# Kernel tuning notes

Measured on AMD Instinct MI355X. Metric: run time of the kernel, lower is better.

Reference implementation:

```python
import jax, jax.numpy as jnp
import numpy as np

N = 32          # agents_num
IN_DIM = 16     # node feature dim (excluding 2 pos cols)
HID = 128
HEADS = 4
OUT = 5
DUEL_H = 256
RADIUS = 0.3
LATENT = HID + HID * HEADS * 2  # 1152
BS = 128


def _lin(k, i, o):
    s = 1.0 / np.sqrt(i)
    return jax.random.uniform(k, (i, o), minval=-s, maxval=s, dtype=jnp.float32)


def setup_inputs() -> dict:
    key = jax.random.key(0)
    ks = jax.random.split(key, 16)
    pos = jax.random.uniform(ks[0], (BS, N, 2))
    feats = jax.random.normal(ks[1], (BS, N, IN_DIM))
    aidx = jax.random.randint(ks[2], (BS,), 0, N).astype(jnp.float32)
    node = jnp.concatenate([pos, feats], axis=-1).reshape(BS, N * (2 + IN_DIM))
    obs = jnp.concatenate([node, aidx[:, None]], axis=1)  # (BS, N*(2+IN_DIM)+1)
    return {
        "obs": obs,
        "enc_w1": _lin(ks[3], IN_DIM, HID), "enc_b1": jnp.zeros((HID,)),
        "enc_w2": _lin(ks[4], HID, HID), "enc_b2": jnp.zeros((HID,)),
        "wl1": _lin(ks[5], HID, HEADS * HID), "wr1": _lin(ks[6], HID, HEADS * HID),
        "att1": jax.random.normal(ks[7], (HEADS, HID)) * 0.1, "bias1": jnp.zeros((HEADS * HID,)),
        "wl2": _lin(ks[8], HID * HEADS, HEADS * HID), "wr2": _lin(ks[9], HID * HEADS, HEADS * HID),
        "att2": jax.random.normal(ks[10], (HEADS, HID)) * 0.1, "bias2": jnp.zeros((HEADS * HID,)),
        "q_w1": _lin(ks[11], LATENT, DUEL_H), "q_b1": jnp.zeros((DUEL_H,)),
        "q_w2": _lin(ks[12], DUEL_H, OUT), "q_b2": jnp.zeros((OUT,)),
        "v_w1": _lin(ks[13], LATENT, DUEL_H), "v_b1": jnp.zeros((DUEL_H,)),
        "v_w2": _lin(ks[14], DUEL_H, 1), "v_b2": jnp.zeros((1,)),
    }


def _gatv2(x, adj, wl, wr, att, bias):
    # Dense-masked GATv2 (PyG semantics: lin_l on source j, lin_r on target i,
    # leaky_relu(x_i + x_j) . att, softmax over neighbors j, aggregate lin_l(x_j)).
    bs, n, _ = x.shape
    gl = (x @ wl).reshape(bs, n, HEADS, HID)  # source transform
    gr = (x @ wr).reshape(bs, n, HEADS, HID)  # target transform
    e = jax.nn.leaky_relu(gr[:, :, None] + gl[:, None, :], 0.2)  # [b, i, j, h, c]
    logits = jnp.einsum('bijhc,hc->bijh', e, att)
    logits = jnp.where(adj[..., None], logits, -jnp.inf)  # diag always True (self loops)
    alpha = jax.nn.softmax(logits, axis=2)
    out = jnp.einsum('bijh,bjhc->bihc', alpha, gl).reshape(bs, n, HEADS * HID)
    return out + bias


def reference(obs, enc_w1, enc_b1, enc_w2, enc_b2,
              wl1, wr1, att1, bias1, wl2, wr2, att2, bias2,
              q_w1, q_b1, q_w2, q_b2, v_w1, v_b1, v_w2, v_b2):
    bs = obs.shape[0]
    node = obs[:, :-1].reshape(bs, N, 2 + IN_DIM)
    pos, feats = node[..., :2], node[..., 2:]
    aidx = jnp.clip(obs[:, -1], 0, N - 1).astype(jnp.int32)

    # radius_graph (per-graph, loop=False) + GATv2 add_self_loops => diag True
    d2 = jnp.sum((pos[:, :, None] - pos[:, None, :]) ** 2, axis=-1)  # [bs, N, N]
    adj = (d2 < RADIUS ** 2) | jnp.eye(N, dtype=bool)

    # encoder MLP then ReLU (as in forward)
    h = jax.nn.relu(feats @ enc_w1 + enc_b1)
    x = jax.nn.relu(h @ enc_w2 + enc_b2)  # [bs, N, HID]

    b = jnp.arange(bs)
    x1 = x[b, aidx]  # [bs, HID]

    x = jax.nn.relu(_gatv2(x, adj, wl1, wr1, att1, bias1))  # [bs, N, HID*HEADS]
    x2 = x[b, aidx]

    x = jax.nn.relu(_gatv2(x, adj, wl2, wr2, att2, bias2))
    x3 = x[b, aidx]

    x_cat = jnp.concatenate([x1, x2, x3], axis=1)  # [bs, LATENT]

    q = jax.nn.relu(x_cat @ q_w1 + q_b1) @ q_w2 + q_b2  # [bs, OUT]
    v = jax.nn.relu(x_cat @ v_w1 + v_b1) @ v_w2 + v_b2  # [bs, 1]
    return q - q.mean(axis=1, keepdims=True) + v
```

## Files before the change

kernel.cpp:

```cpp
#include <hip/hip_runtime.h>
#include <hip/hip_bf16.h>

typedef unsigned int uint_t;
typedef unsigned short ushort_t;
typedef __attribute__((ext_vector_type(8))) short short8;
typedef __attribute__((ext_vector_type(4))) float floatx4;

__device__ __forceinline__ float4 fma4(float4 a, float s, float4 w){
  a.x += s*w.x; a.y += s*w.y; a.z += s*w.z; a.w += s*w.w; return a;
}
__device__ __forceinline__ float4 relu4(float4 a){
  return make_float4(fmaxf(a.x,0.f),fmaxf(a.y,0.f),fmaxf(a.z,0.f),fmaxf(a.w,0.f));
}
__device__ __forceinline__ unsigned bf16rne(float f){
  unsigned u = __float_as_uint(f);
  return (u + 0x7fffu + ((u>>16)&1u)) >> 16;
}
__device__ __forceinline__ uint_t packbf(float f){
  unsigned hb = bf16rne(f);
  float hf = __uint_as_float(hb<<16);
  unsigned lb = bf16rne(f - hf);
  return (hb<<16) | lb;
}
__device__ __forceinline__ uint4 pack4(float4 v){
  uint4 u; u.x=packbf(v.x); u.y=packbf(v.y); u.z=packbf(v.z); u.w=packbf(v.w); return u;
}
__device__ __forceinline__ float unpk(uint_t u){
  return __uint_as_float(u & 0xffff0000u) + __uint_as_float(u<<16);
}
#define UNPACK8(u0,u1,hi,lo) \
  hi[0]=(short)(u0.x>>16); lo[0]=(short)u0.x; \
  hi[1]=(short)(u0.y>>16); lo[1]=(short)u0.y; \
  hi[2]=(short)(u0.z>>16); lo[2]=(short)u0.z; \
  hi[3]=(short)(u0.w>>16); lo[3]=(short)u0.w; \
  hi[4]=(short)(u1.x>>16); lo[4]=(short)u1.x; \
  hi[5]=(short)(u1.y>>16); lo[5]=(short)u1.y; \
  hi[6]=(short)(u1.z>>16); lo[6]=(short)u1.z; \
  hi[7]=(short)(u1.w>>16); lo[7]=(short)u1.w;


template<int NKC>
__device__ __forceinline__ void hgemm_body(
    const uint_t* __restrict__ xcatpk,
    const ushort_t* __restrict__ qw1Thi, const ushort_t* __restrict__ qw1Tlo,
    const ushort_t* __restrict__ vw1Thi, const ushort_t* __restrict__ vw1Tlo,
    float* __restrict__ part, int ks, int ct, int t, int k0c, int slot0)
{
  const int w = t>>6, lane = t&63, m = lane&15, quad = lane>>4;
  const ushort_t* Bhi = (ct<4) ? qw1Thi : vw1Thi;
  const int cbl = (ct<4) ? ct*64 : (ct-4)*64;
  const int cbg = (ct<4) ? ct*64 : 256 + (ct-4)*64;
  const int kb = k0c + ks*NKC;
  const uint_t* ap = xcatpk + (size_t)w*18432 + m*32 + quad*8 + (size_t)kb*512;
  const ushort_t* bp0 = Bhi + (size_t)((cbl>>4)+0)*18432 + m*32 + quad*8 + (size_t)kb*512;
  const ushort_t* bp1 = Bhi + (size_t)((cbl>>4)+1)*18432 + m*32 + quad*8 + (size_t)kb*512;
  const ushort_t* bp2 = Bhi + (size_t)((cbl>>4)+2)*18432 + m*32 + quad*8 + (size_t)kb*512;
  const ushort_t* bp3 = Bhi + (size_t)((cbl>>4)+3)*18432 + m*32 + quad*8 + (size_t)kb*512;
  const size_t lod = (size_t)(qw1Tlo - qw1Thi);
  floatx4 acc[4];
  #pragma unroll
  for (int i=0;i<4;i++) acc[i] = (floatx4){0.f,0.f,0.f,0.f};
  #pragma unroll
  for (int kc=0; kc<NKC; kc++){
    const uint4 ua0 = *(const uint4*)(ap);
    const uint4 ua1 = *(const uint4*)(ap+4);
    ap += 512;
    short8 ahi, alo;
    UNPACK8(ua0,ua1,ahi,alo)
    const ushort_t* bps[4] = {bp0, bp1, bp2, bp3};
    #pragma unroll
    for (int nt=0; nt<4; nt++){
      const short8 bh = *(const short8*)(bps[nt] + kc*512);
      const short8 bl = *(const short8*)(bps[nt] + kc*512 + lod);
      acc[nt] = __builtin_amdgcn_mfma_f32_16x16x32_bf16(ahi, bh, acc[nt], 0,0,0);
      acc[nt] = __builtin_amdgcn_mfma_f32_16x16x32_bf16(ahi, bl, acc[nt], 0,0,0);
      acc[nt] = __builtin_amdgcn_mfma_f32_16x16x32_bf16(alo, bh, acc[nt], 0,0,0);
    }
  }
  float* pdst = part + (size_t)(slot0+ks)*65536;
  const int crow0 = w*16 + quad*4;
  #pragma unroll
  for (int nt=0; nt<4; nt++){
    const int col = cbg + nt*16 + m;
    #pragma unroll
    for (int r=0;r<4;r++)
      pdst[(size_t)(crow0 + r)*512 + col] = acc[nt][r];
  }
}

__global__ __launch_bounds__(256) void prep_kernel(
    const float* __restrict__ obs,
    const float* __restrict__ enc_w1, const float* __restrict__ enc_b1,
    const float* __restrict__ enc_w2, const float* __restrict__ enc_b2,
    const float* __restrict__ wl1, const float* __restrict__ wr1,
    const float* __restrict__ wl2, const float* __restrict__ wr2,
    const float* __restrict__ q_w1, const float* __restrict__ v_w1,
    ushort_t* __restrict__ wl1Thi, ushort_t* __restrict__ wl1Tlo,
    ushort_t* __restrict__ wr1Thi, ushort_t* __restrict__ wr1Tlo,
    ushort_t* __restrict__ wl2Thi, ushort_t* __restrict__ wl2Tlo,
    ushort_t* __restrict__ wr2Thi, ushort_t* __restrict__ wr2Tlo,
    ushort_t* __restrict__ qw1Thi, ushort_t* __restrict__ qw1Tlo,
    ushort_t* __restrict__ vw1Thi, ushort_t* __restrict__ vw1Tlo,
    uint_t* __restrict__ xpk, uint_t* __restrict__ xcatpk,
    unsigned* __restrict__ adjw, int* __restrict__ aiw)
{
  const int t = threadIdx.x, bid = blockIdx.x;
  if (bid >= 512){
    __shared__ float sm[32][33];
    const int cw = bid - 512;
    const float* in; ushort_t* ohi; ushort_t* olo; int K, N, tt, ktiles;
    if (cw < 64)       { in=wl1;  ohi=wl1Thi; olo=wl1Tlo; K=128;  N=512; tt=cw;     ktiles=4;  }
    else if (cw < 128) { in=wr1;  ohi=wr1Thi; olo=wr1Tlo; K=128;  N=512; tt=cw-64;  ktiles=4;  }
    else if (cw < 384) { in=wl2;  ohi=wl2Thi; olo=wl2Tlo; K=512;  N=512; tt=cw-128; ktiles=16; }
    else if (cw < 640) { in=wr2;  ohi=wr2Thi; olo=wr2Tlo; K=512;  N=512; tt=cw-384; ktiles=16; }
    else if (cw < 800) { in=q_w1; ohi=qw1Thi; olo=qw1Tlo; K=1152; N=256; tt=cw-640; ktiles=20; }
    else               { in=v_w1; ohi=vw1Thi; olo=vw1Tlo; K=1152; N=256; tt=cw-800; ktiles=20; }
    const int kt = tt % ktiles, nt = tt / ktiles;
    const int r = t>>5, c = t&31;
    #pragma unroll
    for (int i=0;i<4;i++)
      sm[r+i*8][c] = in[(size_t)(kt*32 + r + i*8)*N + nt*32 + c];
    __syncthreads();
    #pragma unroll
    for (int i=0;i<4;i++){
      const int nl = r + i*8;
      const int n  = nt*32 + nl;
      const float f = sm[c][nl];
      const unsigned hb = bf16rne(f);
      const float hf = __uint_as_float(hb<<16);
      const unsigned lb = bf16rne(f - hf);
      const size_t off = (size_t)(n>>4)*(size_t)(16*K) + (size_t)kt*512 + (size_t)(n&15)*32 + c;
      ohi[off] = (ushort_t)hb;
      olo[off] = (ushort_t)lb;
    }
    return;
  }
  __shared__ float s_pos[64];
  __shared__ float s_feats[128];
  __shared__ __align__(16) float s_h[8*132];
  __shared__ int s_ai;
  const int s = bid & 127, g = bid >> 7;
  const float* ob = obs + s*577;

  if (t==0){
    float a = ob[576];
    a = fminf(fmaxf(a, 0.f), 31.f);
    s_ai = (int)a;
    if (g==0) aiw[s] = (int)a;
  }
  if (t < 128){ const int n=t>>4, f=t&15; s_feats[t] = ob[(g*8+n)*18+2+f]; }
  if (g==0 && t>=128 && t<192){ const int u=t-128; s_pos[u] = ob[(u>>1)*18 + (u&1)]; }
  __syncthreads();

  if (g==0 && t < 32){
    const float px = s_pos[2*t], py = s_pos[2*t+1];
    const float R2 = 0.09f;
    unsigned mm = 0u;
    for (int j=0;j<32;j++){
      const float dx = __fsub_rn(px, s_pos[2*j]), dy = __fsub_rn(py, s_pos[2*j+1]);
      const float d2 = __fadd_rn(__fmul_rn(dx,dx), __fmul_rn(dy,dy));
      if (d2 <= R2 || j==t) mm |= (1u<<j);
    }
    adjw[s*32+t] = mm;
  }

  const int n = t>>5, c0 = (t&31)*4;
  {
    float4 a = *(const float4*)(enc_b1+c0);
    #pragma unroll
    for (int f=0; f<16; f++)
      a = fma4(a, s_feats[n*16+f], *(const float4*)(enc_w1 + f*128 + c0));
    *(float4*)&s_h[n*132+c0] = relu4(a);
  }
  __syncthreads();
  {
    float4 a = *(const float4*)(enc_b2+c0);
    #pragma unroll 4
    for (int k=0;k<128;k+=4){
      const float4 hv = *(const float4*)&s_h[n*132+k];
      a = fma4(a, hv.x, *(const float4*)(enc_w2 + (k+0)*128 + c0));
      a = fma4(a, hv.y, *(const float4*)(enc_w2 + (k+1)*128 + c0));
      a = fma4(a, hv.z, *(const float4*)(enc_w2 + (k+2)*128 + c0));
      a = fma4(a, hv.w, *(const float4*)(enc_w2 + (k+3)*128 + c0));
    }
    a = relu4(a);
    const uint4 p = pack4(a);
    const int i = g*8 + n;
    uint_t* xp = xpk + (size_t)(s*2 + (i>>4))*2048 + (c0>>5)*512 + (i&15)*32 + (c0&31);
    *(uint4*)xp = p;
    if (i == s_ai){
      uint_t* xc = xcatpk + (size_t)(s>>4)*18432 + (c0>>5)*512 + (s&15)*32 + (c0&31);
      *(uint4*)xc = p;
    }
  }
}

__global__ __launch_bounds__(512) void pa1_kernel(
    const uint_t* __restrict__ xpk,
    const ushort_t* __restrict__ wl1Thi, const ushort_t* __restrict__ wl1Tlo,
    const ushort_t* __restrict__ wr1Thi, const ushort_t* __restrict__ wr1Tlo,
    const float* __restrict__ att, const float* __restrict__ bias,
    const unsigned* __restrict__ adjw, const int* __restrict__ aiw,
    uint_t* __restrict__ x2pk, uint_t* __restrict__ xcatpk)
{
  __shared__ __align__(16) uint_t s_ax[4096];
  __shared__ __align__(16) float s_gl[32*132];
  __shared__ __align__(16) float s_gr[32*132];
  __shared__ __align__(16) float s_att[128];
  __shared__ __align__(16) float s_b[128];
  __shared__ float s_lg[32*33];
  __shared__ unsigned s_adj[32];
  const int t = threadIdx.x, bid = blockIdx.x;

  const int s = bid & 127, h = bid >> 7;
  const int w = t>>6, lane = t&63, m = lane&15, quad = lane>>4;
  const int mat = w>>2, cpair = w&3;

  if (t < 128){ s_att[t] = att[h*128 + t]; s_b[t] = bias[h*128 + t]; }
  if (t >= 224 && t < 256) s_adj[t-224] = adjw[s*32 + (t-224)];
  const int ai = aiw[s];

  #pragma unroll
  for (int j=0;j<2;j++){
    const int W = t*8 + j*4;
    const int kcl = W>>10, rp = (W>>9)&1, u = W&511;
    const int du = u ^ (((u>>5)&7)<<2);
    *(uint4*)&s_ax[kcl*1024 + rp*512 + du] =
      *(const uint4*)(xpk + (size_t)(s*2+rp)*2048 + (size_t)kcl*512 + u);
  }

  const ushort_t* Bhi = (mat==0) ? wl1Thi : wr1Thi;
  const ushort_t* Blo = (mat==0) ? wl1Tlo : wr1Tlo;
  const int nbase = h*8 + cpair*2;
  const ushort_t* bp0 = Bhi + (size_t)(nbase+0)*2048 + m*32 + quad*8;
  const ushort_t* bp1 = Bhi + (size_t)(nbase+1)*2048 + m*32 + quad*8;
  const size_t lod = (size_t)(Blo - Bhi);
  const int sw = (m*32 + quad*8) ^ ((m&7)<<2);
  floatx4 acc[2][2];
  #pragma unroll
  for (int i=0;i<2;i++)
    #pragma unroll
    for (int j=0;j<2;j++) acc[i][j] = (floatx4){0.f,0.f,0.f,0.f};

  __syncthreads();

  #pragma unroll
  for (int kc=0; kc<4; kc++){
    const uint4 u00 = *(const uint4*)&s_ax[kc*1024 + sw];
    const uint4 u01 = *(const uint4*)&s_ax[kc*1024 + (sw^4)];
    const uint4 u10 = *(const uint4*)&s_ax[kc*1024 + 512 + sw];
    const uint4 u11 = *(const uint4*)&s_ax[kc*1024 + 512 + (sw^4)];
    short8 ahi0, alo0, ahi1, alo1;
    UNPACK8(u00,u01,ahi0,alo0)
    UNPACK8(u10,u11,ahi1,alo1)
    const ushort_t* bps[2] = {bp0, bp1};
    #pragma unroll
    for (int nt=0; nt<2; nt++){
      const short8 bh = *(const short8*)(bps[nt] + kc*512);
      const short8 bl = *(const short8*)(bps[nt] + kc*512 + lod);
      acc[0][nt] = __builtin_amdgcn_mfma_f32_16x16x32_bf16(ahi0, bh, acc[0][nt], 0,0,0);
      acc[0][nt] = __builtin_amdgcn_mfma_f32_16x16x32_bf16(ahi0, bl, acc[0][nt], 0,0,0);
      acc[0][nt] = __builtin_amdgcn_mfma_f32_16x16x32_bf16(alo0, bh, acc[0][nt], 0,0,0);
      acc[1][nt] = __builtin_amdgcn_mfma_f32_16x16x32_bf16(ahi1, bh, acc[1][nt], 0,0,0);
      acc[1][nt] = __builtin_amdgcn_mfma_f32_16x16x32_bf16(ahi1, bl, acc[1][nt], 0,0,0);
      acc[1][nt] = __builtin_amdgcn_mfma_f32_16x16x32_bf16(alo1, bh, acc[1][nt], 0,0,0);
    }
  }
  {
    float* dst = mat ? s_gr : s_gl;
    const int colbase = cpair*32;
    #pragma unroll
    for (int nt=0; nt<2; nt++){
      const int col = colbase + nt*16 + m;
      #pragma unroll
      for (int r=0;r<4;r++){
        dst[(quad*4+r)*132 + col]      = acc[0][nt][r];
        dst[(16+quad*4+r)*132 + col]   = acc[1][nt][r];
      }
    }
  }
  __syncthreads();

  {
    const int i = t>>4, jb = t&15;
    float lacc[2] = {0.f,0.f};
    for (int c=0;c<128;c+=4){
      const float4 g = *(const float4*)&s_gr[i*132+c];
      const float4 a = *(const float4*)&s_att[c];
      #pragma unroll
      for (int mm=0;mm<2;mm++){
        const float4 gj = *(const float4*)&s_gl[(jb+16*mm)*132 + c];
        float ex = g.x+gj.x; ex = fmaxf(ex, 0.2f*ex);
        float ey = g.y+gj.y; ey = fmaxf(ey, 0.2f*ey);
        float ez = g.z+gj.z; ez = fmaxf(ez, 0.2f*ez);
        float ew = g.w+gj.w; ew = fmaxf(ew, 0.2f*ew);
        lacc[mm] += ex*a.x + ey*a.y + ez*a.z + ew*a.w;
      }
    }
    s_lg[i*33 + jb]      = lacc[0];
    s_lg[i*33 + jb + 16] = lacc[1];
  }
  __syncthreads();

  #pragma unroll
  for (int rnd=0; rnd<2; rnd++){
    const int i = rnd*16 + (t>>5), j = t&31;
    const float lg = s_lg[i*33+j];
    const bool ok = (s_adj[i]>>j)&1u;
    float v = ok ? lg : -3.0e38f;
    #pragma unroll
    for (int d_=16; d_; d_>>=1) v = fmaxf(v, __shfl_xor(v, d_, 32));
    const float e = ok ? __expf(lg - v) : 0.f;
    float sum = e;
    #pragma unroll
    for (int d_=16; d_; d_>>=1) sum += __shfl_xor(sum, d_, 32);
    s_lg[i*33+j] = e / sum;
  }
  __syncthreads();

  {
    const int i = t>>4, c0 = (t&15)*8;
    float4 o0 = make_float4(0.f,0.f,0.f,0.f), o1 = o0;
    for (int j=0;j<32;j++){
      const float al = s_lg[i*33+j];
      o0 = fma4(o0, al, *(const float4*)&s_gl[j*132 + c0]);
      o1 = fma4(o1, al, *(const float4*)&s_gl[j*132 + c0 + 4]);
    }
    const float4 b0 = *(const float4*)&s_b[c0];
    const float4 b1 = *(const float4*)&s_b[c0+4];
    o0 = relu4(make_float4(o0.x+b0.x, o0.y+b0.y, o0.z+b0.z, o0.w+b0.w));
    o1 = relu4(make_float4(o1.x+b1.x, o1.y+b1.y, o1.z+b1.z, o1.w+b1.w));
    const uint4 p0 = pack4(o0), p1 = pack4(o1);
    const int kb = h*128 + c0;
    uint_t* xp = x2pk + (size_t)(s*2 + (i>>4))*8192 + (kb>>5)*512 + (i&15)*32 + (kb&31);
    *(uint4*)&xp[0] = p0;
    *(uint4*)&xp[4] = p1;
    if (i == ai){
      const int kk = 128 + kb;
      uint_t* tp = xcatpk + (size_t)(s>>4)*18432 + (kk>>5)*512 + (s&15)*32 + (kk&31);
      *(uint4*)&tp[0] = p0;
      *(uint4*)&tp[4] = p1;
    }
  }
}

__global__ __launch_bounds__(512) void gr2_kernel(
    const uint_t* __restrict__ xcatpk,
    const ushort_t* __restrict__ wr2Thi, const ushort_t* __restrict__ wr2Tlo,
    const ushort_t* __restrict__ qw1Thi, const ushort_t* __restrict__ qw1Tlo,
    const ushort_t* __restrict__ vw1Thi, const ushort_t* __restrict__ vw1Tlo,
    float* __restrict__ hpart, float* __restrict__ GR)
{
  const int t = threadIdx.x, bid = blockIdx.x;
  if (bid >= 32){
    const int hk = bid - 32;
    hgemm_body<5>(xcatpk, qw1Thi, qw1Tlo, vw1Thi, vw1Tlo, hpart, hk>>3, hk&7, t, 0, 0);
    return;
  }
  const int w = t>>6, lane = t&63, m = lane&15, quad = lane>>4;
  const uint_t* ap = xcatpk + (size_t)w*18432 + m*32 + quad*8 + (size_t)4*512;
  const ushort_t* bp = wr2Thi + (size_t)bid*8192 + m*32 + quad*8;
  const size_t lod = (size_t)(wr2Tlo - wr2Thi);
  floatx4 acc = (floatx4){0.f,0.f,0.f,0.f};
  #pragma unroll 4
  for (int kc=0; kc<16; kc++){
    const uint4 ua0 = *(const uint4*)(ap + kc*512);
    const uint4 ua1 = *(const uint4*)(ap + kc*512 + 4);
    short8 ahi, alo;
    UNPACK8(ua0,ua1,ahi,alo)
    const short8 bh = *(const short8*)(bp + kc*512);
    const short8 bl = *(const short8*)(bp + kc*512 + lod);
    acc = __builtin_amdgcn_mfma_f32_16x16x32_bf16(ahi, bh, acc, 0,0,0);
    acc = __builtin_amdgcn_mfma_f32_16x16x32_bf16(ahi, bl, acc, 0,0,0);
    acc = __builtin_amdgcn_mfma_f32_16x16x32_bf16(alo, bh, acc, 0,0,0);
  }
  const int row0 = w*16 + quad*4, col = bid*16 + m;
  #pragma unroll
  for (int r=0;r<4;r++)
    GR[(size_t)(row0 + r)*512 + col] = acc[r];
}

__global__ __launch_bounds__(512) void pa2_kernel(
    const uint_t* __restrict__ x2pk,
    const ushort_t* __restrict__ wl2Thi, const ushort_t* __restrict__ wl2Tlo,
    const float* __restrict__ GR,
    const float* __restrict__ att2, const float* __restrict__ bias2,
    const unsigned* __restrict__ adjw, const int* __restrict__ aiw,
    float* __restrict__ X3)
{
  __shared__ __align__(16) uint_t s_a[8192];
  __shared__ __align__(16) float s_gl[32*132];
  __shared__ __align__(16) float s_p2[128];
  __shared__ __align__(16) float s_at[128];
  __shared__ __align__(16) float s_bb[128];
  __shared__ float s_lg[32];
  __shared__ float s_al[32];
  const int t = threadIdx.x, bid = blockIdx.x;
  const int s = bid & 127, h = bid >> 7;
  const int w = t>>6, lane = t&63, m = lane&15, quad = lane>>4;
  (void)lane;
  const int ai = aiw[s];
  const unsigned arow = adjw[s*32+ai];

  if (t < 128){
    s_p2[t] = GR[(size_t)s*512 + h*128 + t];
    s_at[t] = att2[h*128+t];
    s_bb[t] = bias2[h*128+t];
  }

  const ushort_t* bq = wl2Thi + (size_t)(h*8 + w)*8192 + m*32 + quad*8;
  const size_t lod = (size_t)(wl2Tlo - wl2Thi);
  const int sw = (m*32 + quad*8) ^ ((m&7)<<2);
  floatx4 acc0 = (floatx4){0.f,0.f,0.f,0.f}, acc1 = acc0;

  #pragma unroll
  for (int half=0; half<2; half++){
    #pragma unroll
    for (int j=0;j<4;j++){
      const int W = t*16 + j*4;
      const int kcl = W>>10, rp = (W>>9)&1, u = W&511;
      const int du = u ^ (((u>>5)&7)<<2);
      *(uint4*)&s_a[kcl*1024 + rp*512 + du] =
        *(const uint4*)(x2pk + (size_t)(s*2+rp)*8192 + (size_t)(half*8+kcl)*512 + u);
    }
    __syncthreads();
    #pragma unroll 4
    for (int kcl=0; kcl<8; kcl++){
      const int kc = half*8 + kcl;
      const uint4 u00 = *(const uint4*)&s_a[kcl*1024 + sw];
      const uint4 u01 = *(const uint4*)&s_a[kcl*1024 + (sw^4)];
      const uint4 u10 = *(const uint4*)&s_a[kcl*1024 + 512 + sw];
      const uint4 u11 = *(const uint4*)&s_a[kcl*1024 + 512 + (sw^4)];
      short8 ahi0, alo0, ahi1, alo1;
      UNPACK8(u00,u01,ahi0,alo0)
      UNPACK8(u10,u11,ahi1,alo1)
      const short8 bh = *(const short8*)(bq + kc*512);
      const short8 bl = *(const short8*)(bq + kc*512 + lod);
      acc0 = __builtin_amdgcn_mfma_f32_16x16x32_bf16(ahi0, bh, acc0, 0,0,0);
      acc0 = __builtin_amdgcn_mfma_f32_16x16x32_bf16(ahi0, bl, acc0, 0,0,0);
      acc0 = __builtin_amdgcn_mfma_f32_16x16x32_bf16(alo0, bh, acc0, 0,0,0);
      acc1 = __builtin_amdgcn_mfma_f32_16x16x32_bf16(ahi1, bh, acc1, 0,0,0);
      acc1 = __builtin_amdgcn_mfma_f32_16x16x32_bf16(ahi1, bl, acc1, 0,0,0);
      acc1 = __builtin_amdgcn_mfma_f32_16x16x32_bf16(alo1, bh, acc1, 0,0,0);
    }
    __syncthreads();
  }
  {
    const int col = w*16 + m;
    #pragma unroll
    for (int r=0;r<4;r++){
      s_gl[(quad*4+r)*132 + col]    = acc0[r];
      s_gl[(16+quad*4+r)*132 + col] = acc1[r];
    }
  }
  __syncthreads();

  if (t < 256){
    const int j = t>>3, pq = t&7;
    float sum = 0.f;
    #pragma unroll
    for (int q=0;q<4;q++){
      const int c = pq*16 + q*4;
      const float4 g = *(const float4*)&s_gl[j*132 + c];
      const float4 r = *(const float4*)&s_p2[c];
      const float4 a = *(const float4*)&s_at[c];
      float e0 = r.x+g.x; e0 = fmaxf(e0, 0.2f*e0);
      float e1 = r.y+g.y; e1 = fmaxf(e1, 0.2f*e1);
      float e2 = r.z+g.z; e2 = fmaxf(e2, 0.2f*e2);
      float e3 = r.w+g.w; e3 = fmaxf(e3, 0.2f*e3);
      sum += e0*a.x + e1*a.y + e2*a.z + e3*a.w;
    }
    sum += __shfl_xor(sum,1,64);
    sum += __shfl_xor(sum,2,64);
    sum += __shfl_xor(sum,4,64);
    if (pq==0) s_lg[j] = sum;
  }
  __syncthreads();
  if (t < 32){
    const float lg = s_lg[t];
    const bool ok = (arow>>t)&1u;
    float v = ok ? lg : -3.0e38f;
    #pragma unroll
    for (int d_=16; d_; d_>>=1) v = fmaxf(v, __shfl_xor(v, d_, 32));
    const float e = ok ? __expf(lg - v) : 0.f;
    float sm = e;
    #pragma unroll
    for (int d_=16; d_; d_>>=1) sm += __shfl_xor(sm, d_, 32);
    s_al[t] = e / sm;
  }
  __syncthreads();
  if (t < 128){
    float acc2 = 0.f;
    #pragma unroll 8
    for (int j=0;j<32;j++) acc2 += s_al[j] * s_gl[j*132 + t];
    X3[(size_t)s*512 + h*128 + t] = fmaxf(acc2 + s_bb[t], 0.f);
  }
}

__global__ __launch_bounds__(512) void hepi_kernel(
    const float* __restrict__ X3, const float* __restrict__ hpart,
    const float* __restrict__ q_w1, const float* __restrict__ q_b1,
    const float* __restrict__ q_w2, const float* __restrict__ q_b2,
    const float* __restrict__ v_w1, const float* __restrict__ v_b1,
    const float* __restrict__ v_w2, const float* __restrict__ v_b2,
    float* __restrict__ out)
{
  __shared__ __align__(16) float s_x3[512];
  __shared__ float s_p6[8*6];
  const int t = threadIdx.x, s = blockIdx.x;
  const int w = t>>6, lane = t&63;

  s_x3[t] = X3[(size_t)s*512 + t];
  __syncthreads();

  float val;
  {
    const int col = t & 255;
    float acc = (t < 256) ? q_b1[col] : v_b1[col];
    #pragma unroll
    for (int ks=0; ks<4; ks++)
      acc += hpart[(size_t)ks*65536 + (size_t)s*512 + t];
    const float* Wp = ((t < 256) ? q_w1 : v_w1) + (size_t)640*256 + col;
    #pragma unroll 8
    for (int k=0;k<512;k++) acc += s_x3[k] * Wp[(size_t)k*256];
    val = fmaxf(acc, 0.f);
  }

  float p[6];
  #pragma unroll
  for (int o=0;o<6;o++) p[o] = 0.f;
  if (t < 256){
    #pragma unroll
    for (int o=0;o<5;o++) p[o] = val * q_w2[t*5+o];
  } else {
    p[5] = val * v_w2[t-256];
  }
  #pragma unroll
  for (int d_=32; d_; d_>>=1){
    #pragma unroll
    for (int o=0;o<6;o++) p[o] += __shfl_xor(p[o], d_, 64);
  }
  if (lane==0){
    #pragma unroll
    for (int o=0;o<6;o++) s_p6[w*6+o] = p[o];
  }
  __syncthreads();
  if (t < 6){
    float v = 0.f;
    #pragma unroll
    for (int ww=0; ww<8; ww++) v += s_p6[ww*6 + t];
    s_p6[t] = v;
  }
  __syncthreads();
  if (t < 5){
    const float q0 = s_p6[0]+q_b2[0], q1 = s_p6[1]+q_b2[1], q2 = s_p6[2]+q_b2[2],
                q3 = s_p6[3]+q_b2[3], q4 = s_p6[4]+q_b2[4];
    const float mean = (q0+q1+q2+q3+q4) / 5.0f;
    const float v = s_p6[5] + v_b2[0];
    const float qt = (t==0?q0:t==1?q1:t==2?q2:t==3?q3:q4);
    out[s*5+t] = qt - mean + v;
  }
}

extern "C" void kernel_launch(void* const* d_in, const int* in_sizes, int n_in,
                              void* d_out, int out_size, void* d_ws, size_t ws_size,
                              hipStream_t stream) {
  (void)n_in; (void)out_size; (void)ws_size;
  const float* obs    = (const float*)d_in[0];
  const float* enc_w1 = (const float*)d_in[1];
  const float* enc_b1 = (const float*)d_in[2];
  const float* enc_w2 = (const float*)d_in[3];
  const float* enc_b2 = (const float*)d_in[4];
  const float* wl1    = (const float*)d_in[5];
  const float* wr1    = (const float*)d_in[6];
  const float* att1   = (const float*)d_in[7];
  const float* bias1  = (const float*)d_in[8];
  const float* wl2    = (const float*)d_in[9];
  const float* wr2    = (const float*)d_in[10];
  const float* att2   = (const float*)d_in[11];
  const float* bias2  = (const float*)d_in[12];
  const float* q_w1   = (const float*)d_in[13];
  const float* q_b1   = (const float*)d_in[14];
  const float* q_w2   = (const float*)d_in[15];
  const float* q_b2   = (const float*)d_in[16];
  const float* v_w1   = (const float*)d_in[17];
  const float* v_b1   = (const float*)d_in[18];
  const float* v_w2   = (const float*)d_in[19];
  const float* v_b2   = (const float*)d_in[20];

  char* ws = (char*)d_ws;
  uint_t*   x_pk    = (uint_t*)  (ws + 0);
  uint_t*   xcat_pk = (uint_t*)  (ws + 2097152);
  unsigned* adjw    = (unsigned*)(ws + 2686976);
  int*      aiw     = (int*)     (ws + 2703360);
  uint_t*   x2_pk   = (uint_t*)  (ws + 2703872);
  ushort_t* wl1Thi  = (ushort_t*)(ws + 11092480);
  ushort_t* wl1Tlo  = (ushort_t*)(ws + 11223552);
  ushort_t* wr1Thi  = (ushort_t*)(ws + 11354624);
  ushort_t* wr1Tlo  = (ushort_t*)(ws + 11485696);
  ushort_t* wl2Thi  = (ushort_t*)(ws + 11616768);
  ushort_t* wl2Tlo  = (ushort_t*)(ws + 12141056);
  ushort_t* qw1Thi  = (ushort_t*)(ws + 12665344);
  ushort_t* qw1Tlo  = (ushort_t*)(ws + 13255168);
  ushort_t* vw1Thi  = (ushort_t*)(ws + 13844992);
  ushort_t* vw1Tlo  = (ushort_t*)(ws + 14434816);
  ushort_t* wr2Thi  = (ushort_t*)(ws + 15024640);
  ushort_t* wr2Tlo  = (ushort_t*)(ws + 15548928);
  float*    GR      = (float*)   (ws + 16073216);
  float*    hpart   = (float*)   (ws + 16335360);
  float*    X3      = (float*)   (ws + 17383936);

  prep_kernel<<<512 + 960, 256, 0, stream>>>(obs, enc_w1, enc_b1, enc_w2, enc_b2,
      wl1, wr1, wl2, wr2, q_w1, v_w1,
      wl1Thi, wl1Tlo, wr1Thi, wr1Tlo, wl2Thi, wl2Tlo, wr2Thi, wr2Tlo,
      qw1Thi, qw1Tlo, vw1Thi, vw1Tlo,
      x_pk, xcat_pk, adjw, aiw);

  pa1_kernel<<<512, 512, 0, stream>>>(x_pk, wl1Thi, wl1Tlo, wr1Thi, wr1Tlo,
      att1, bias1, adjw, aiw, x2_pk, xcat_pk);

  gr2_kernel<<<64, 512, 0, stream>>>(xcat_pk, wr2Thi, wr2Tlo,
      qw1Thi, qw1Tlo, vw1Thi, vw1Tlo, hpart, GR);

  pa2_kernel<<<512, 512, 0, stream>>>(x2_pk, wl2Thi, wl2Tlo, GR,
      att2, bias2, adjw, aiw, X3);

  hepi_kernel<<<128, 512, 0, stream>>>(X3, hpart,
      q_w1, q_b1, q_w2, q_b2, v_w1, v_b1, v_w2, v_b2,
      (float*)d_out);
}
```

Measured before the change: 174.9 us.

## Fuse target-transform GEMM and head-split q/v layer into layer-2 attention kernel

Removes the separate gr2 kernel. Each pa2 block now computes its own 16-row tile of the wr2 target transform from xcat staged in shared memory. The 32 hgemm blocks move into the pa2 grid, so one launch and a global round trip disappear. The per-head slice of the q/v first-layer matvec also moves into pa2, writing per-head partials that a slimmer hepi kernel only sums. The cost is redundant work: each of the 16 samples in a row tile recomputes the same GR tile, and the fp32 weight reads for the q/v matvec are spread across many blocks.

```diff
diff --git a/kernel.cpp b/kernel.cpp
--- a/kernel.cpp
+++ b/kernel.cpp
@@ -344,49 +344,16 @@
   }
 }
 
-__global__ __launch_bounds__(512) void gr2_kernel(
-    const uint_t* __restrict__ xcatpk,
+__global__ __launch_bounds__(512) void pa2_kernel(
+    const uint_t* __restrict__ x2pk, const uint_t* __restrict__ xcatpk,
+    const ushort_t* __restrict__ wl2Thi, const ushort_t* __restrict__ wl2Tlo,
     const ushort_t* __restrict__ wr2Thi, const ushort_t* __restrict__ wr2Tlo,
     const ushort_t* __restrict__ qw1Thi, const ushort_t* __restrict__ qw1Tlo,
     const ushort_t* __restrict__ vw1Thi, const ushort_t* __restrict__ vw1Tlo,
-    float* __restrict__ hpart, float* __restrict__ GR)
-{
-  const int t = threadIdx.x, bid = blockIdx.x;
-  if (bid >= 32){
-    const int hk = bid - 32;
-    hgemm_body<5>(xcatpk, qw1Thi, qw1Tlo, vw1Thi, vw1Tlo, hpart, hk>>3, hk&7, t, 0, 0);
-    return;
-  }
-  const int w = t>>6, lane = t&63, m = lane&15, quad = lane>>4;
-  const uint_t* ap = xcatpk + (size_t)w*18432 + m*32 + quad*8 + (size_t)4*512;
-  const ushort_t* bp = wr2Thi + (size_t)bid*8192 + m*32 + quad*8;
-  const size_t lod = (size_t)(wr2Tlo - wr2Thi);
-  floatx4 acc = (floatx4){0.f,0.f,0.f,0.f};
-  #pragma unroll 4
-  for (int kc=0; kc<16; kc++){
-    const uint4 ua0 = *(const uint4*)(ap + kc*512);
-    const uint4 ua1 = *(const uint4*)(ap + kc*512 + 4);
-    short8 ahi, alo;
-    UNPACK8(ua0,ua1,ahi,alo)
-    const short8 bh = *(const short8*)(bp + kc*512);
-    const short8 bl = *(const short8*)(bp + kc*512 + lod);
-    acc = __builtin_amdgcn_mfma_f32_16x16x32_bf16(ahi, bh, acc, 0,0,0);
-    acc = __builtin_amdgcn_mfma_f32_16x16x32_bf16(ahi, bl, acc, 0,0,0);
-    acc = __builtin_amdgcn_mfma_f32_16x16x32_bf16(alo, bh, acc, 0,0,0);
-  }
-  const int row0 = w*16 + quad*4, col = bid*16 + m;
-  #pragma unroll
-  for (int r=0;r<4;r++)
-    GR[(size_t)(row0 + r)*512 + col] = acc[r];
-}
-
-__global__ __launch_bounds__(512) void pa2_kernel(
-    const uint_t* __restrict__ x2pk,
-    const ushort_t* __restrict__ wl2Thi, const ushort_t* __restrict__ wl2Tlo,
-    const float* __restrict__ GR,
     const float* __restrict__ att2, const float* __restrict__ bias2,
     const unsigned* __restrict__ adjw, const int* __restrict__ aiw,
-    float* __restrict__ X3)
+    const float* __restrict__ q_w1, const float* __restrict__ v_w1,
+    float* __restrict__ hpart, float* __restrict__ hp3)
 {
   __shared__ __align__(16) uint_t s_a[8192];
   __shared__ __align__(16) float s_gl[32*132];
@@ -396,21 +363,61 @@
   __shared__ float s_lg[32];
   __shared__ float s_al[32];
   const int t = threadIdx.x, bid = blockIdx.x;
+
+  if (bid >= 512){
+    const int hk = bid - 512;
+    hgemm_body<5>(xcatpk, qw1Thi, qw1Tlo, vw1Thi, vw1Tlo, hpart, hk>>3, hk&7, t, 0, 0);
+    return;
+  }
+
   const int s = bid & 127, h = bid >> 7;
   const int w = t>>6, lane = t&63, m = lane&15, quad = lane>>4;
   (void)lane;
   const int ai = aiw[s];
   const unsigned arow = adjw[s*32+ai];
-
-  if (t < 128){
-    s_p2[t] = GR[(size_t)s*512 + h*128 + t];
-    s_at[t] = att2[h*128+t];
-    s_bb[t] = bias2[h*128+t];
-  }
+  const int sw = (m*32 + quad*8) ^ ((m&7)<<2);
+
+  if (t < 128){ s_at[t] = att2[h*128+t]; s_bb[t] = bias2[h*128+t]; }
+
+  {
+    const int rt = s >> 4;
+    #pragma unroll
+    for (int j=0;j<4;j++){
+      const int W = t*16 + j*4;
+      const int kcl = W>>9, u = W&511;
+      const int du = u ^ (((u>>5)&7)<<2);
+      *(uint4*)&s_a[kcl*512 + du] =
+        *(const uint4*)(xcatpk + (size_t)rt*18432 + (size_t)(4+kcl)*512 + u);
+    }
+  }
+  __syncthreads();
+  {
+    const int ct = h*8 + w;
+    const ushort_t* bp = wr2Thi + (size_t)ct*8192 + m*32 + quad*8;
+    const size_t lodr = (size_t)(wr2Tlo - wr2Thi);
+    floatx4 acc = (floatx4){0.f,0.f,0.f,0.f};
+    #pragma unroll 4
+    for (int kc=0; kc<16; kc++){
+      const uint4 ua0 = *(const uint4*)&s_a[kc*512 + sw];
+      const uint4 ua1 = *(const uint4*)&s_a[kc*512 + (sw^4)];
+      short8 ahi, alo;
+      UNPACK8(ua0,ua1,ahi,alo)
+      const short8 bh = *(const short8*)(bp + kc*512);
+      const short8 bl = *(const short8*)(bp + kc*512 + lodr);
+      acc = __builtin_amdgcn_mfma_f32_16x16x32_bf16(ahi, bh, acc, 0,0,0);
+      acc = __builtin_amdgcn_mfma_f32_16x16x32_bf16(ahi, bl, acc, 0,0,0);
+      acc = __builtin_amdgcn_mfma_f32_16x16x32_bf16(alo, bh, acc, 0,0,0);
+    }
+    #pragma unroll
+    for (int r=0;r<4;r++)
+      s_gl[(quad*4+r)*132 + w*16 + m] = acc[r];
+  }
+  __syncthreads();
+  if (t < 128) s_p2[t] = s_gl[(s&15)*132 + t];
+  __syncthreads();
 
   const ushort_t* bq = wl2Thi + (size_t)(h*8 + w)*8192 + m*32 + quad*8;
   const size_t lod = (size_t)(wl2Tlo - wl2Thi);
-  const int sw = (m*32 + quad*8) ^ ((m&7)<<2);
   floatx4 acc0 = (floatx4){0.f,0.f,0.f,0.f}, acc1 = acc0;
 
   #pragma unroll
@@ -493,70 +500,64 @@
     float acc2 = 0.f;
     #pragma unroll 8
     for (int j=0;j<32;j++) acc2 += s_al[j] * s_gl[j*132 + t];
-    X3[(size_t)s*512 + h*128 + t] = fmaxf(acc2 + s_bb[t], 0.f);
-  }
-}
-
-__global__ __launch_bounds__(512) void hepi_kernel(
-    const float* __restrict__ X3, const float* __restrict__ hpart,
-    const float* __restrict__ q_w1, const float* __restrict__ q_b1,
-    const float* __restrict__ q_w2, const float* __restrict__ q_b2,
-    const float* __restrict__ v_w1, const float* __restrict__ v_b1,
-    const float* __restrict__ v_w2, const float* __restrict__ v_b2,
+    s_p2[t] = fmaxf(acc2 + s_bb[t], 0.f);
+  }
+  __syncthreads();
+
+  {
+    const float* Wm = (t < 256) ? q_w1 : v_w1;
+    const int col = t & 255;
+    const float* wp = Wm + (size_t)(640 + h*128)*256 + col;
+    float acc3 = 0.f;
+    #pragma unroll 8
+    for (int k=0;k<128;k++) acc3 += s_p2[k] * wp[(size_t)k*256];
+    hp3[((size_t)h*128 + s)*512 + t] = acc3;
+  }
+}
+
+__global__ __launch_bounds__(256) void hepi_kernel(
+    const float* __restrict__ hpart, const float* __restrict__ hp3,
+    const float* __restrict__ q_b1, const float* __restrict__ q_w2, const float* __restrict__ q_b2,
+    const float* __restrict__ v_b1, const float* __restrict__ v_w2, const float* __restrict__ v_b2,
     float* __restrict__ out)
 {
-  __shared__ __align__(16) float s_x3[512];
-  __shared__ float s_p6[8*6];
+  __shared__ float s_p[4*6];
   const int t = threadIdx.x, s = blockIdx.x;
+  float hq = q_b1[t], hv = v_b1[t];
+  #pragma unroll
+  for (int ks=0; ks<4; ks++){
+    hq += hpart[(size_t)ks*65536 + (size_t)s*512 + t];
+    hv += hpart[(size_t)ks*65536 + (size_t)s*512 + 256 + t];
+  }
+  #pragma unroll
+  for (int h=0; h<4; h++){
+    hq += hp3[((size_t)h*128 + s)*512 + t];
+    hv += hp3[((size_t)h*128 + s)*512 + 256 + t];
+  }
+  hq = fmaxf(hq, 0.f);
+  hv = fmaxf(hv, 0.f);
+  float p[6];
+  #pragma unroll
+  for (int o=0;o<5;o++) p[o] = hq * q_w2[t*5+o];
+  p[5] = hv * v_w2[t];
+  #pragma unroll
+  for (int d_=32; d_; d_>>=1){
+    #pragma unroll
+    for (int o=0;o<6;o++) p[o] += __shfl_xor(p[o], d_, 64);
+  }
   const int w = t>>6, lane = t&63;
-
-  s_x3[t] = X3[(size_t)s*512 + t];
-  __syncthreads();
-
-  float val;
-  {
-    const int col = t & 255;
-    float acc = (t < 256) ? q_b1[col] : v_b1[col];
-    #pragma unroll
-    for (int ks=0; ks<4; ks++)
-      acc += hpart[(size_t)ks*65536 + (size_t)s*512 + t];
-    const float* Wp = ((t < 256) ? q_w1 : v_w1) + (size_t)640*256 + col;
-    #pragma unroll 8
-    for (int k=0;k<512;k++) acc += s_x3[k] * Wp[(size_t)k*256];
-    val = fmaxf(acc, 0.f);
-  }
-
-  float p[6];
-  #pragma unroll
-  for (int o=0;o<6;o++) p[o] = 0.f;
-  if (t < 256){
-    #pragma unroll
-    for (int o=0;o<5;o++) p[o] = val * q_w2[t*5+o];
-  } else {
-    p[5] = val * v_w2[t-256];
-  }
-  #pragma unroll
-  for (int d_=32; d_; d_>>=1){
-    #pragma unroll
-    for (int o=0;o<6;o++) p[o] += __shfl_xor(p[o], d_, 64);
-  }
   if (lane==0){
     #pragma unroll
-    for (int o=0;o<6;o++) s_p6[w*6+o] = p[o];
-  }
-  __syncthreads();
-  if (t < 6){
-    float v = 0.f;
-    #pragma unroll
-    for (int ww=0; ww<8; ww++) v += s_p6[ww*6 + t];
-    s_p6[t] = v;
-  }
+    for (int o=0;o<6;o++) s_p[w*6+o] = p[o];
+  }
+  __syncthreads();
+  if (t < 6) s_p[t] = s_p[t] + s_p[6+t] + s_p[12+t] + s_p[18+t];
   __syncthreads();
   if (t < 5){
-    const float q0 = s_p6[0]+q_b2[0], q1 = s_p6[1]+q_b2[1], q2 = s_p6[2]+q_b2[2],
-                q3 = s_p6[3]+q_b2[3], q4 = s_p6[4]+q_b2[4];
+    const float q0 = s_p[0]+q_b2[0], q1 = s_p[1]+q_b2[1], q2 = s_p[2]+q_b2[2],
+                q3 = s_p[3]+q_b2[3], q4 = s_p[4]+q_b2[4];
     const float mean = (q0+q1+q2+q3+q4) / 5.0f;
-    const float v = s_p6[5] + v_b2[0];
+    const float v = s_p[5] + v_b2[0];
     const float qt = (t==0?q0:t==1?q1:t==2?q2:t==3?q3:q4);
     out[s*5+t] = qt - mean + v;
   }
@@ -606,9 +607,8 @@
   ushort_t* vw1Tlo  = (ushort_t*)(ws + 14434816);
   ushort_t* wr2Thi  = (ushort_t*)(ws + 15024640);
   ushort_t* wr2Tlo  = (ushort_t*)(ws + 15548928);
-  float*    GR      = (float*)   (ws + 16073216);
-  float*    hpart   = (float*)   (ws + 16335360);
-  float*    X3      = (float*)   (ws + 17383936);
+  float*    hpart   = (float*)   (ws + 16073216);
+  float*    hp3     = (float*)   (ws + 17121792);
 
   prep_kernel<<<512 + 960, 256, 0, stream>>>(obs, enc_w1, enc_b1, enc_w2, enc_b2,
       wl1, wr1, wl2, wr2, q_w1, v_w1,
@@ -619,13 +619,13 @@
   pa1_kernel<<<512, 512, 0, stream>>>(x_pk, wl1Thi, wl1Tlo, wr1Thi, wr1Tlo,
       att1, bias1, adjw, aiw, x2_pk, xcat_pk);
 
-  gr2_kernel<<<64, 512, 0, stream>>>(xcat_pk, wr2Thi, wr2Tlo,
-      qw1Thi, qw1Tlo, vw1Thi, vw1Tlo, hpart, GR);
-
-  pa2_kernel<<<512, 512, 0, stream>>>(x2_pk, wl2Thi, wl2Tlo, GR,
-      att2, bias2, adjw, aiw, X3);
-
-  hepi_kernel<<<128, 512, 0, stream>>>(X3, hpart,
-      q_w1, q_b1, q_w2, q_b2, v_w1, v_b1, v_w2, v_b2,
+  pa2_kernel<<<512 + 32, 512, 0, stream>>>(x2_pk, xcat_pk,
+      wl2Thi, wl2Tlo, wr2Thi, wr2Tlo,
+      qw1Thi, qw1Tlo, vw1Thi, vw1Tlo,
+      att2, bias2, adjw, aiw, q_w1, v_w1,
+      hpart, hp3);
+
+  hepi_kernel<<<128, 256, 0, stream>>>(hpart, hp3,
+      q_b1, q_w2, q_b2, v_b1, v_w2, v_b2,
       (float*)d_out);
 }
```

Result: faster. 161.8 us (median of 3 runs) (-7.5%).
